# Kernel tuning notes

Hardware: AMD Instinct MI355X
Metric: run time of the kernel (lower is better)

## Reference

```python
import jax, jax.numpy as jnp
import numpy as np

N = 50000          # nodes
E = 800000         # edges (before self-loops)
IN_DIM = 128
HID = 64           # hidden_dim (per-head out channels)
HEADS = 2
NL = 3             # num_layers of GATConv
CH = HEADS * HID   # 128, per-layer node feature width
LSTM_H = (2 * CH) // 2  # 128, PyG JumpingKnowledge lstm hidden size (num_layers=2)
NEG_SLOPE = 0.2


def setup_inputs() -> dict:
    key = jax.random.key(0)
    ks = jax.random.split(key, 24)
    r = lambda i, shape, s=0.1: jax.random.normal(ks[i], shape, dtype=jnp.float32) * s
    return {
        "x": jax.random.normal(ks[0], (N, IN_DIM), dtype=jnp.float32),
        "edge_index": jax.random.randint(ks[1], (2, E), 0, N),
        "W1": r(2, (CH, IN_DIM)),
        "att1_src": r(3, (HEADS, HID)),
        "att1_dst": r(4, (HEADS, HID)),
        "b1": r(5, (CH,)),
        "Ws": r(6, (NL - 1, CH, CH)),
        "atts_src": r(7, (NL - 1, HEADS, HID)),
        "atts_dst": r(8, (NL - 1, HEADS, HID)),
        "bs": r(9, (NL - 1, CH)),
        "lstm_Wih": r(10, (2, 4 * LSTM_H, CH)),
        "lstm_Whh": r(11, (2, 4 * LSTM_H, LSTM_H)),
        "lstm_bih": r(12, (2, 4 * LSTM_H)),
        "lstm_bhh": r(13, (2, 4 * LSTM_H)),
        "jk_att_w": r(14, (1, 2 * LSTM_H)),
        "jk_att_b": r(15, (1,)),
        "lin1_w": r(16, (HID, CH)),
        "lin1_b": r(17, (HID,)),
        "lin2_w": r(18, (HID, HID + IN_DIM)),
        "lin2_b": r(19, (HID,)),
        "out_w": r(20, (6, HID)),
        "out_b": r(21, (6,)),
    }


def _gat(x, src, dst, W, a_src, a_dst, b):
    # PyG GATConv: linear -> per-head attention logits -> segment softmax over
    # incoming edges -> weighted scatter-add -> concat heads + bias.
    xp = (x @ W.T).reshape(N, HEADS, HID)          # [N,H,C]
    es = jnp.sum(xp * a_src, -1)                   # [N,H]
    ed = jnp.sum(xp * a_dst, -1)                   # [N,H]
    e = jax.nn.leaky_relu(es[src] + ed[dst], NEG_SLOPE)  # [E,H]
    m = jax.ops.segment_max(e, dst, num_segments=N)
    ex = jnp.exp(e - m[dst])
    s = jax.ops.segment_sum(ex, dst, num_segments=N)
    alpha = ex / s[dst]                            # [E,H]
    out = jax.ops.segment_sum(xp[src] * alpha[..., None], dst, num_segments=N)
    return out.reshape(N, CH) + b


def _lstm_dir(seq, Wih, Whh, bih, bhh, reverse):
    # seq: [L, N, CH]; torch gate order (i, f, g, o)
    def step(carry, xt):
        h, c = carry
        g = xt @ Wih.T + bih + h @ Whh.T + bhh
        i, f, gg, o = jnp.split(g, 4, axis=-1)
        c = jax.nn.sigmoid(f) * c + jax.nn.sigmoid(i) * jnp.tanh(gg)
        h = jax.nn.sigmoid(o) * jnp.tanh(c)
        return (h, c), h
    z = jnp.zeros((seq.shape[1], LSTM_H), seq.dtype)
    _, hs = jax.lax.scan(step, (z, z), seq, reverse=reverse)
    return hs  # [L, N, LSTM_H]


def reference(x, edge_index, W1, att1_src, att1_dst, b1, Ws, atts_src, atts_dst, bs,
              lstm_Wih, lstm_Whh, lstm_bih, lstm_bhh, jk_att_w, jk_att_b,
              lin1_w, lin1_b, lin2_w, lin2_b, out_w, out_b):
    loops = jnp.arange(N)
    src = jnp.concatenate([edge_index[0], loops])  # PyG adds self-loops
    dst = jnp.concatenate([edge_index[1], loops])

    h = _gat(x, src, dst, W1, att1_src, att1_dst, b1)  # conv1: no relu on xs[0]
    xs = [h]
    for l in range(NL - 1):
        h = jax.nn.relu(_gat(h, src, dst, Ws[l], atts_src[l], atts_dst[l], bs[l]))
        xs.append(h)

    # JumpingKnowledge 'lstm': biLSTM over layer axis, attention-weighted sum.
    X = jnp.stack(xs, axis=0)                       # [L, N, CH]
    hf = _lstm_dir(X, lstm_Wih[0], lstm_Whh[0], lstm_bih[0], lstm_bhh[0], False)
    hb = _lstm_dir(X, lstm_Wih[1], lstm_Whh[1], lstm_bih[1], lstm_bhh[1], True)
    hcat = jnp.concatenate([hf, hb], -1)            # [L, N, 2*LSTM_H]
    score = (hcat @ jk_att_w.T + jk_att_b)[..., 0]  # [L, N]
    alpha = jax.nn.softmax(score, axis=0)
    jk = jnp.sum(X * alpha[..., None], axis=0)      # [N, CH]

    h1 = jax.nn.relu(jk @ lin1_w.T + lin1_b)        # dropout is identity (eval)
    h2 = jax.nn.relu(jnp.concatenate([h1, x], axis=1) @ lin2_w.T + lin2_b)
    logits = h2 @ out_w.T + out_b
    return jax.nn.log_softmax(logits, axis=1)
```

## Files before the change

### kernel.cpp

```cpp
#include <hip/hip_runtime.h>
#include <math.h>

#define CDIV(a,b) (((a)+(b)-1)/(b))

typedef __attribute__((ext_vector_type(8))) short bfrag;
typedef __attribute__((ext_vector_type(4))) float ffrag;

__device__ inline unsigned short f2bf(float f) {
    unsigned int u = __float_as_uint(f);
    return (unsigned short)((u + 0x7fffu + ((u >> 16) & 1u)) >> 16);
}
__device__ inline float bf2f(unsigned short u) {
    return __uint_as_float(((unsigned int)u) << 16);
}
__device__ inline float sigf(float x) {
    return __builtin_amdgcn_rcpf(1.f + __expf(-x));
}
__device__ inline float tanhfast(float x) {
    float t = __expf(-2.f * fabsf(x));
    float r = (1.f - t) * __builtin_amdgcn_rcpf(1.f + t);
    return copysignf(r, x);
}
__device__ inline int hoff(int row, int k) {
    int sw = ((k >> 3) ^ row) & 15;
    return row * 128 + sw * 8 + (k & 7);
}

__global__ void zero_i32(int* __restrict__ p, int n) {
    int i = blockIdx.x * 256 + threadIdx.x;
    if (i < n) p[i] = 0;
}
__global__ void init_score_k(float* __restrict__ sc, const float* __restrict__ b, int n) {
    int i = blockIdx.x * 256 + threadIdx.x;
    if (i < n) sc[i] = b[0];
}
__global__ void convert_bf_k(const float* __restrict__ src, unsigned short* __restrict__ dst, int n) {
    int i = blockIdx.x * 256 + threadIdx.x;
    if (i < n) dst[i] = f2bf(src[i]);
}

__global__ void hist_k(const int* __restrict__ ei, int E, int ET, int* __restrict__ deg) {
    int e = blockIdx.x * 256 + threadIdx.x;
    if (e >= ET) return;
    int d = (e < E) ? ei[E + e] : e - E;
    atomicAdd(deg + d, 1);
}

__global__ __launch_bounds__(256)
void scan1_k(const int* __restrict__ deg, int* __restrict__ row_ptr,
             int* __restrict__ part, int Nn) {
    __shared__ int ls[256];
    int t = threadIdx.x;
    int base = blockIdx.x * 1024 + t * 4;
    int v[4];
    #pragma unroll
    for (int j = 0; j < 4; ++j) v[j] = (base + j < Nn) ? deg[base + j] : 0;
    int s = v[0] + v[1] + v[2] + v[3];
    ls[t] = s;
    __syncthreads();
    for (int off = 1; off < 256; off <<= 1) {
        int o = (t >= off) ? ls[t - off] : 0;
        __syncthreads();
        ls[t] += o;
        __syncthreads();
    }
    int run = ls[t] - s;
    if (t == 255) part[blockIdx.x] = ls[255];
    #pragma unroll
    for (int j = 0; j < 4; ++j) {
        if (base + j < Nn) row_ptr[base + j] = run;
        run += v[j];
    }
}
__global__ void scan2_k(int* __restrict__ part, int nb) {
    int lane = threadIdx.x;
    int v = (lane < nb) ? part[lane] : 0;
    int orig = v;
    for (int off = 1; off < 64; off <<= 1) {
        int o = __shfl_up(v, off);
        if (lane >= off) v += o;
    }
    if (lane < nb) part[lane] = v - orig;
}
__global__ void scan3_k(const int* __restrict__ part, int* __restrict__ row_ptr,
                        int* __restrict__ cursor, int Nn) {
    int i = blockIdx.x * 256 + threadIdx.x;
    if (i >= Nn) return;
    int v = row_ptr[i] + part[i >> 10];
    row_ptr[i] = v;
    cursor[i] = v;
}

__global__ void fill_k(const int* __restrict__ ei, int E, int ET,
                       int* __restrict__ cursor, int* __restrict__ csr_src) {
    int e = blockIdx.x * 256 + threadIdx.x;
    if (e >= ET) return;
    int s, d;
    if (e < E) { s = ei[e]; d = ei[E + e]; } else { s = e - E; d = s; }
    int pos = atomicAdd(cursor + d, 1);
    csr_src[pos] = s;
}

__global__ void pack_w_k(const float* __restrict__ Wih, const float* __restrict__ Whh,
                         const float* __restrict__ bih, const float* __restrict__ bhh,
                         unsigned short* __restrict__ Wp, float* __restrict__ bsum) {
    int i = blockIdx.x * 256 + threadIdx.x;
    if (i < 1024) bsum[i] = bih[i] + bhh[i];
    if (i >= 2 * 512 * 256) return;
    int k = i & 255, j = (i >> 8) & 511, d = i >> 17;
    float v = (k < 128) ? Wih[((size_t)d * 512 + j) * 128 + k]
                        : Whh[((size_t)d * 512 + j) * 128 + (k - 128)];
    Wp[i] = f2bf(v);
}

__global__ void pack_wb_k(const float* __restrict__ W1, const float* __restrict__ Ws,
                          const float* __restrict__ l1w, const float* __restrict__ l2w,
                          unsigned short* __restrict__ wb) {
    int i = blockIdx.x * 256 + threadIdx.x;
    if (i >= 69632) return;
    float v;
    if (i < 16384)      v = W1[i];
    else if (i < 49152) v = Ws[i - 16384];
    else if (i < 57344) v = l1w[i - 49152];
    else                v = l2w[i - 57344];
    wb[i] = f2bf(v);
}

template<int NT, int K, int K1, bool RELU, bool FUSE, bool BFOUT>
__global__ __launch_bounds__(256)
void gemm_mfma_k(const unsigned short* __restrict__ A1, const unsigned short* __restrict__ A2,
                 int ldA2, const unsigned short* __restrict__ Wb, const float* __restrict__ bias,
                 unsigned short* __restrict__ Cb, float* __restrict__ Cf,
                 const float* __restrict__ asl, const float* __restrict__ adl,
                 float* __restrict__ es, float* __restrict__ ed, int M)
{
    int tid = threadIdx.x;
    int wv = tid >> 6, lane = tid & 63;
    int col = lane & 15, kg = lane >> 4;
    int row0 = blockIdx.x * 64 + wv * 16;
    int mrow = row0 + col;
    bool mok = mrow < M;

    ffrag acc[NT];
    #pragma unroll
    for (int t = 0; t < NT; ++t) acc[t] = (ffrag){0.f, 0.f, 0.f, 0.f};

    #pragma unroll
    for (int ks = 0; ks < K / 32; ++ks) {
        int kk = ks * 32 + kg * 8;
        bfrag a = (bfrag){0,0,0,0,0,0,0,0};
        if (mok) {
            if (kk < K1) a = *(const bfrag*)(A1 + (size_t)mrow * K1 + kk);
            else         a = *(const bfrag*)(A2 + (size_t)mrow * ldA2 + (kk - K1));
        }
        #pragma unroll
        for (int t = 0; t < NT; ++t) {
            bfrag b = *(const bfrag*)(Wb + (size_t)(t * 16 + col) * K + kk);
            acc[t] = __builtin_amdgcn_mfma_f32_16x16x32_bf16(a, b, acc[t], 0, 0, 0);
        }
    }

    #pragma unroll
    for (int r = 0; r < 4; ++r) {
        int n = row0 + kg * 4 + r;
        bool ok = n < M;
        float e0 = 0.f, e1 = 0.f, d0 = 0.f, d1 = 0.f;
        #pragma unroll
        for (int t = 0; t < NT; ++t) {
            float v = acc[t][r];
            if (FUSE) {
                int ch = t * 16 + col;
                if (t < NT / 2) { e0 = fmaf(v, asl[ch], e0); d0 = fmaf(v, adl[ch], d0); }
                else            { e1 = fmaf(v, asl[ch], e1); d1 = fmaf(v, adl[ch], d1); }
            }
            if (bias) v += bias[t * 16 + col];
            if (RELU) v = fmaxf(v, 0.f);
            if (ok) {
                if (BFOUT) Cb[(size_t)n * (NT * 16) + t * 16 + col] = f2bf(v);
                else       Cf[(size_t)n * (NT * 16) + t * 16 + col] = v;
            }
        }
        if (FUSE) {
            #pragma unroll
            for (int mk = 1; mk < 16; mk <<= 1) {
                e0 += __shfl_xor(e0, mk); e1 += __shfl_xor(e1, mk);
                d0 += __shfl_xor(d0, mk); d1 += __shfl_xor(d1, mk);
            }
            if (col == 0 && ok) {
                es[n * 2] = e0; es[n * 2 + 1] = e1;
                ed[n * 2] = d0; ed[n * 2 + 1] = d1;
            }
        }
    }
}

__global__ __launch_bounds__(256)
void gat_agg_k(const int* __restrict__ csr_src, const int* __restrict__ row_ptr,
               const int* __restrict__ deg,
               const unsigned short* __restrict__ xpb, const float* __restrict__ es,
               const float* __restrict__ ed, const float* __restrict__ bias,
               unsigned short* __restrict__ out, int Nn, int relu)
{
    int wid = (blockIdx.x * 256 + threadIdx.x) >> 6;
    int lane = threadIdx.x & 63;
    if (wid >= Nn) return;
    int n = wid;
    int beg = row_ptr[n];
    int dn = deg[n];
    float2 edv = *(const float2*)(ed + n * 2);

    int   src_c = 0;
    float z0_c = 0.f, z1_c = 0.f;
    float m0 = -3e38f, m1 = -3e38f, s0 = 0.f, s1 = 0.f;
    for (int i = lane; i < dn; i += 64) {
        int s = csr_src[beg + i];
        float2 e2 = *(const float2*)(es + s * 2);
        float z0 = e2.x + edv.x; z0 = z0 > 0.f ? z0 : 0.2f * z0;
        float z1 = e2.y + edv.y; z1 = z1 > 0.f ? z1 : 0.2f * z1;
        if (i == lane) { src_c = s; z0_c = z0; z1_c = z1; }
        float nm0 = fmaxf(m0, z0);
        s0 = s0 * __expf(m0 - nm0) + __expf(z0 - nm0); m0 = nm0;
        float nm1 = fmaxf(m1, z1);
        s1 = s1 * __expf(m1 - nm1) + __expf(z1 - nm1); m1 = nm1;
    }
    #pragma unroll
    for (int off = 32; off; off >>= 1) {
        float om0 = __shfl_xor(m0, off), os0 = __shfl_xor(s0, off);
        float nm0 = fmaxf(m0, om0);
        s0 = s0 * __expf(m0 - nm0) + os0 * __expf(om0 - nm0); m0 = nm0;
        float om1 = __shfl_xor(m1, off), os1 = __shfl_xor(s1, off);
        float nm1 = fmaxf(m1, om1);
        s1 = s1 * __expf(m1 - nm1) + os1 * __expf(om1 - nm1); m1 = nm1;
    }
    float inv0 = 1.f / s0, inv1 = 1.f / s1;

    float acc0 = 0.f, acc1 = 0.f;
    if (dn <= 64) {
        #pragma unroll 8
        for (int i = 0; i < dn; ++i) {
            int s = __shfl(src_c, i);
            float a0 = __expf(__shfl(z0_c, i) - m0) * inv0;
            float a1 = __expf(__shfl(z1_c, i) - m1) * inv1;
            float aw = (lane < 32) ? a0 : a1;
            unsigned int u = *(const unsigned int*)(xpb + (size_t)s * 128 + 2 * lane);
            acc0 = fmaf(bf2f((unsigned short)(u & 0xffff)), aw, acc0);
            acc1 = fmaf(bf2f((unsigned short)(u >> 16)), aw, acc1);
        }
    } else {
        for (int i = 0; i < dn; ++i) {
            int s = csr_src[beg + i];
            float2 e2 = *(const float2*)(es + s * 2);
            float z0 = e2.x + edv.x; z0 = z0 > 0.f ? z0 : 0.2f * z0;
            float z1 = e2.y + edv.y; z1 = z1 > 0.f ? z1 : 0.2f * z1;
            float a0 = __expf(z0 - m0) * inv0;
            float a1 = __expf(z1 - m1) * inv1;
            float aw = (lane < 32) ? a0 : a1;
            unsigned int u = *(const unsigned int*)(xpb + (size_t)s * 128 + 2 * lane);
            acc0 = fmaf(bf2f((unsigned short)(u & 0xffff)), aw, acc0);
            acc1 = fmaf(bf2f((unsigned short)(u >> 16)), aw, acc1);
        }
    }
    float2 bb = *(const float2*)(bias + 2 * lane);
    float v0 = acc0 + bb.x;
    float v1 = acc1 + bb.y;
    if (relu) { v0 = fmaxf(v0, 0.f); v1 = fmaxf(v1, 0.f); }
    unsigned int o = (unsigned int)f2bf(v0) | ((unsigned int)f2bf(v1) << 16);
    *(unsigned int*)(out + (size_t)n * 128 + 2 * lane) = o;
}

__global__ __launch_bounds__(512)
void lstm_all_k(const unsigned short* __restrict__ X0, const unsigned short* __restrict__ X1,
                const unsigned short* __restrict__ X2,
                const unsigned short* __restrict__ WpB, const float* __restrict__ bsumB,
                const float* __restrict__ jkw, float* __restrict__ score, int Nn, int ntiles)
{
    __shared__ unsigned short h_lds[2][32 * 128];
    int dir = blockIdx.y;
    const unsigned short* Xs0 = dir ? X2 : X0;
    const unsigned short* Xs2 = dir ? X0 : X2;
    const unsigned short* Wp = WpB + (size_t)dir * 512 * 256;
    const float* bsum = bsumB + dir * 512;
    const float* wsc = jkw + dir * 128;

    int tid = threadIdx.x;
    int wv = tid >> 6, lane = tid & 63;
    int col = lane & 15, kg = lane >> 4;
    int t0 = dir ? 2 : 0;
    int kch = 16 * wv + col;
    float bi = bsum[kch], bf_ = bsum[128 + kch];
    float bg = bsum[256 + kch], bo = bsum[384 + kch];
    float wk = wsc[kch];

    bfrag wreg[4][8];
    #pragma unroll
    for (int g = 0; g < 4; ++g) {
        const unsigned short* wrow = Wp + (size_t)(16 * (8 * g + wv) + col) * 256;
        #pragma unroll
        for (int ks = 0; ks < 8; ++ks)
            wreg[g][ks] = *(const bfrag*)(wrow + ks * 32 + kg * 8);
    }

    for (int tile = blockIdx.x; tile < ntiles; tile += gridDim.x) {
        int node0 = tile * 32;
        float c[2][4] = {};

        #pragma unroll
        for (int i = 0; i < 3; ++i) {
            int t = (i == 0) ? t0 : ((i == 1) ? 1 : (2 - t0));
            const unsigned short* Xt = (i == 0) ? Xs0 : ((i == 1) ? X1 : Xs2);
            const unsigned short* h_rd = h_lds[(i + 1) & 1];
            unsigned short* h_wr = h_lds[i & 1];

            ffrag acc[2][4];
            #pragma unroll
            for (int nt = 0; nt < 2; ++nt)
                #pragma unroll
                for (int g = 0; g < 4; ++g) acc[nt][g] = (ffrag){0.f, 0.f, 0.f, 0.f};

            #pragma unroll
            for (int ks = 0; ks < 4; ++ks) {
                int kk = ks * 32 + kg * 8;
                bfrag a0 = *(const bfrag*)(Xt + (size_t)(node0 + col) * 128 + kk);
                bfrag a1 = *(const bfrag*)(Xt + (size_t)(node0 + 16 + col) * 128 + kk);
                #pragma unroll
                for (int g = 0; g < 4; ++g) {
                    acc[0][g] = __builtin_amdgcn_mfma_f32_16x16x32_bf16(a0, wreg[g][ks], acc[0][g], 0, 0, 0);
                    acc[1][g] = __builtin_amdgcn_mfma_f32_16x16x32_bf16(a1, wreg[g][ks], acc[1][g], 0, 0, 0);
                }
            }

            if (i > 0) {
                #pragma unroll
                for (int ks = 4; ks < 8; ++ks) {
                    int kh = (ks - 4) * 32 + kg * 8;
                    bfrag ah0 = *(const bfrag*)&h_rd[hoff(col, kh)];
                    bfrag ah1 = *(const bfrag*)&h_rd[hoff(16 + col, kh)];
                    #pragma unroll
                    for (int g = 0; g < 4; ++g) {
                        acc[0][g] = __builtin_amdgcn_mfma_f32_16x16x32_bf16(ah0, wreg[g][ks], acc[0][g], 0, 0, 0);
                        acc[1][g] = __builtin_amdgcn_mfma_f32_16x16x32_bf16(ah1, wreg[g][ks], acc[1][g], 0, 0, 0);
                    }
                }
            }

            #pragma unroll
            for (int nt = 0; nt < 2; ++nt) {
                #pragma unroll
                for (int r = 0; r < 4; ++r) {
                    float gi = acc[nt][0][r] + bi;
                    float gf = acc[nt][1][r] + bf_;
                    float gg = acc[nt][2][r] + bg;
                    float go = acc[nt][3][r] + bo;
                    float si = sigf(gi);
                    float sf = sigf(gf);
                    float so = sigf(go);
                    float tg = tanhfast(gg);
                    float cn = sf * c[nt][r] + si * tg;
                    float hn = so * tanhfast(cn);
                    c[nt][r] = cn;
                    int nl = nt * 16 + kg * 4 + r;
                    h_wr[hoff(nl, kch)] = f2bf(hn);
                    float v = hn * wk;
                    #pragma unroll
                    for (int mk = 1; mk < 16; mk <<= 1) v += __shfl_xor(v, mk);
                    if (col == 0) {
                        int n = node0 + nl;
                        if (n < Nn) atomicAdd(&score[(size_t)t * Nn + n], v);
                    }
                }
            }
            __syncthreads();
        }
    }
}

__global__ void jk_combine_k(const float* __restrict__ score, const unsigned short* __restrict__ x0,
                             const unsigned short* __restrict__ x1, const unsigned short* __restrict__ x2,
                             unsigned short* __restrict__ jkb, int N_) {
    int gid = blockIdx.x * 256 + threadIdx.x;
    int n = gid >> 5;
    if (n >= N_) return;
    int c = (gid & 31) * 4;
    float s0 = score[n], s1 = score[N_ + n], s2 = score[2*N_ + n];
    float mx = fmaxf(s0, fmaxf(s1, s2));
    float e0 = __expf(s0 - mx), e1 = __expf(s1 - mx), e2 = __expf(s2 - mx);
    float inv = 1.f / (e0 + e1 + e2);
    float a0 = e0 * inv, a1 = e1 * inv, a2 = e2 * inv;
    size_t off = (size_t)n * 128 + c;
    ushort4 u0 = *(const ushort4*)(x0 + off);
    ushort4 u1 = *(const ushort4*)(x1 + off);
    ushort4 u2 = *(const ushort4*)(x2 + off);
    ushort4 o;
    o.x = f2bf(a0*bf2f(u0.x) + a1*bf2f(u1.x) + a2*bf2f(u2.x));
    o.y = f2bf(a0*bf2f(u0.y) + a1*bf2f(u1.y) + a2*bf2f(u2.y));
    o.z = f2bf(a0*bf2f(u0.z) + a1*bf2f(u1.z) + a2*bf2f(u2.z));
    o.w = f2bf(a0*bf2f(u0.w) + a1*bf2f(u1.w) + a2*bf2f(u2.w));
    *(ushort4*)(jkb + off) = o;
}

__global__ void final_out_k(const float* __restrict__ h2, const float* __restrict__ ow,
                            const float* __restrict__ ob, float* __restrict__ out, int N_) {
    int n = blockIdx.x * 256 + threadIdx.x;
    if (n >= N_) return;
    float l[6];
    #pragma unroll
    for (int j = 0; j < 6; ++j) l[j] = ob[j];
    for (int c = 0; c < 64; c += 4) {
        float4 h4 = *(const float4*)(h2 + (size_t)n * 64 + c);
        #pragma unroll
        for (int j = 0; j < 6; ++j) {
            l[j] += h4.x * ow[j*64 + c + 0] + h4.y * ow[j*64 + c + 1]
                  + h4.z * ow[j*64 + c + 2] + h4.w * ow[j*64 + c + 3];
        }
    }
    float mx = l[0];
    #pragma unroll
    for (int j = 1; j < 6; ++j) mx = fmaxf(mx, l[j]);
    float se = 0.f;
    #pragma unroll
    for (int j = 0; j < 6; ++j) se += __expf(l[j] - mx);
    float ls = logf(se) + mx;
    #pragma unroll
    for (int j = 0; j < 6; ++j) out[(size_t)n * 6 + j] = l[j] - ls;
}

extern "C" void kernel_launch(void* const* d_in, const int* in_sizes, int n_in,
                              void* d_out, int out_size, void* d_ws, size_t ws_size,
                              hipStream_t stream) {
    const float* x   = (const float*)d_in[0];
    const int*   ei  = (const int*)d_in[1];
    const float* W1  = (const float*)d_in[2];
    const float* a1s = (const float*)d_in[3];
    const float* a1d = (const float*)d_in[4];
    const float* b1  = (const float*)d_in[5];
    const float* Ws  = (const float*)d_in[6];
    const float* ass = (const float*)d_in[7];
    const float* asd = (const float*)d_in[8];
    const float* bs  = (const float*)d_in[9];
    const float* Wih = (const float*)d_in[10];
    const float* Whh = (const float*)d_in[11];
    const float* bih = (const float*)d_in[12];
    const float* bhh = (const float*)d_in[13];
    const float* jkw = (const float*)d_in[14];
    const float* jkb_b = (const float*)d_in[15];
    const float* l1w = (const float*)d_in[16];
    const float* l1b = (const float*)d_in[17];
    const float* l2w = (const float*)d_in[18];
    const float* l2b = (const float*)d_in[19];
    const float* ow  = (const float*)d_in[20];
    const float* ob  = (const float*)d_in[21];
    float* out = (float*)d_out;

    int Nn = in_sizes[0] / 128;
    int E  = in_sizes[1] / 2;
    int ET = E + Nn;
    size_t Np = ((size_t)Nn + 63) & ~(size_t)63;
    size_t Fp = Np * 128;

    float* w = (float*)d_ws;
    float* es    = w;
    float* ed    = es + 2*Nn;
    float* score = ed + 2*Nn;
    float* bsum  = score + 3*Nn;
    float* h2    = bsum + 1024;
    unsigned short* xb   = (unsigned short*)(h2 + (size_t)Nn*64);
    unsigned short* xpb  = xb + Fp;
    unsigned short* xsb0 = xpb + Fp;
    unsigned short* xsb1 = xsb0 + Fp;
    unsigned short* xsb2 = xsb1 + Fp;
    unsigned short* h1b  = xsb2 + Fp;
    unsigned short* Wp   = h1b + Fp;
    unsigned short* wb   = Wp + 2*512*256;
    int* deg     = (int*)(wb + 69632);
    int* row_ptr = deg + Nn;
    int* cursor  = row_ptr + Nn;
    int* part    = cursor + Nn;
    int* csr_src = part + 64;
    unsigned short* jkb = xpb;

    int nb1 = CDIV(Nn, 1024);
    zero_i32<<<CDIV(Nn, 256), 256, 0, stream>>>(deg, Nn);
    hist_k<<<CDIV(ET, 256), 256, 0, stream>>>(ei, E, ET, deg);
    scan1_k<<<nb1, 256, 0, stream>>>(deg, row_ptr, part, Nn);
    scan2_k<<<1, 64, 0, stream>>>(part, nb1);
    scan3_k<<<CDIV(Nn, 256), 256, 0, stream>>>(part, row_ptr, cursor, Nn);
    fill_k<<<CDIV(ET, 256), 256, 0, stream>>>(ei, E, ET, cursor, csr_src);

    pack_w_k<<<CDIV(2*512*256, 256), 256, 0, stream>>>(Wih, Whh, bih, bhh, Wp, bsum);
    pack_wb_k<<<CDIV(69632, 256), 256, 0, stream>>>(W1, Ws, l1w, l2w, wb);
    convert_bf_k<<<CDIV(Nn*128, 256), 256, 0, stream>>>(x, xb, Nn*128);

    unsigned short* xsb_arr[3] = {xsb0, xsb1, xsb2};
    int gblk = CDIV(Nn, 64);

    for (int l = 0; l < 3; ++l) {
        const float* asl = (l == 0) ? a1s : ass + (size_t)(l-1) * 128;
        const float* adl = (l == 0) ? a1d : asd + (size_t)(l-1) * 128;
        const float* bl  = (l == 0) ? b1  : bs  + (size_t)(l-1) * 128;
        const unsigned short* Ain = (l == 0) ? xb : xsb_arr[l-1];
        const unsigned short* Wbl = wb + (size_t)l * 16384;
        gemm_mfma_k<8,128,128,false,true,true><<<gblk, 256, 0, stream>>>(
            Ain, Ain, 128, Wbl, nullptr, xpb, nullptr, asl, adl, es, ed, Nn);
        gat_agg_k<<<CDIV(Nn, 4), 256, 0, stream>>>(csr_src, row_ptr, deg, xpb, es, ed, bl,
                                                   xsb_arr[l], Nn, l > 0);
    }

    init_score_k<<<CDIV(3*Nn, 256), 256, 0, stream>>>(score, jkb_b, 3*Nn);
    int ntiles = CDIV(Nn, 32);
    int gx = ntiles < 128 ? ntiles : 128;
    lstm_all_k<<<dim3(gx, 2), 512, 0, stream>>>(xsb0, xsb1, xsb2, Wp, bsum, jkw, score, Nn, ntiles);

    jk_combine_k<<<CDIV(Nn*32, 256), 256, 0, stream>>>(score, xsb0, xsb1, xsb2, jkb, Nn);
    gemm_mfma_k<4,128,128,true,false,true><<<gblk, 256, 0, stream>>>(
        jkb, jkb, 128, wb + 49152, l1b, h1b, nullptr, nullptr, nullptr, nullptr, nullptr, Nn);
    gemm_mfma_k<4,192,64,true,false,false><<<gblk, 256, 0, stream>>>(
        h1b, xb, 128, wb + 57344, l2b, nullptr, h2, nullptr, nullptr, nullptr, nullptr, Nn);
    final_out_k<<<CDIV(Nn, 256), 256, 0, stream>>>(h2, ow, ob, out, Nn);
}
```

Measured before the change: 623.1 us.

## Fuse prep kernels, hoist attention exp out of aggregation loop, widen LSTM grid

Three unrelated changes. The weight packing and input bf16 conversion kernels are merged into one launch to cut launch overhead. In the low-degree GAT aggregation path, each lane computes its own attention weight once and the loop broadcasts it with shuffles, replacing a per-edge exp on every lane. The LSTM grid x-dimension cap rises from 128 to 256 blocks so more tiles run concurrently.

```diff
diff --git a/kernel.cpp b/kernel.cpp
--- a/kernel.cpp
+++ b/kernel.cpp
@@ -34,9 +34,35 @@
     int i = blockIdx.x * 256 + threadIdx.x;
     if (i < n) sc[i] = b[0];
 }
-__global__ void convert_bf_k(const float* __restrict__ src, unsigned short* __restrict__ dst, int n) {
+
+__global__ void prep_k(const float* __restrict__ Wih, const float* __restrict__ Whh,
+                       const float* __restrict__ bih, const float* __restrict__ bhh,
+                       unsigned short* __restrict__ Wp, float* __restrict__ bsum,
+                       const float* __restrict__ W1, const float* __restrict__ Ws,
+                       const float* __restrict__ l1w, const float* __restrict__ l2w,
+                       unsigned short* __restrict__ wb,
+                       const float* __restrict__ x, unsigned short* __restrict__ xb, int nx) {
     int i = blockIdx.x * 256 + threadIdx.x;
-    if (i < n) dst[i] = f2bf(src[i]);
+    if (i < 1024) bsum[i] = bih[i] + bhh[i];
+    if (i < 262144) {
+        int k = i & 255, j = (i >> 8) & 511, d = i >> 17;
+        float v = (k < 128) ? Wih[((size_t)d * 512 + j) * 128 + k]
+                            : Whh[((size_t)d * 512 + j) * 128 + (k - 128)];
+        Wp[i] = f2bf(v);
+        return;
+    }
+    int i2 = i - 262144;
+    if (i2 < 69632) {
+        float v;
+        if (i2 < 16384)      v = W1[i2];
+        else if (i2 < 49152) v = Ws[i2 - 16384];
+        else if (i2 < 57344) v = l1w[i2 - 49152];
+        else                 v = l2w[i2 - 57344];
+        wb[i2] = f2bf(v);
+        return;
+    }
+    int i3 = i2 - 69632;
+    if (i3 < nx) xb[i3] = f2bf(x[i3]);
 }
 
 __global__ void hist_k(const int* __restrict__ ei, int E, int ET, int* __restrict__ deg) {
@@ -99,31 +125,6 @@
     if (e < E) { s = ei[e]; d = ei[E + e]; } else { s = e - E; d = s; }
     int pos = atomicAdd(cursor + d, 1);
     csr_src[pos] = s;
-}
-
-__global__ void pack_w_k(const float* __restrict__ Wih, const float* __restrict__ Whh,
-                         const float* __restrict__ bih, const float* __restrict__ bhh,
-                         unsigned short* __restrict__ Wp, float* __restrict__ bsum) {
-    int i = blockIdx.x * 256 + threadIdx.x;
-    if (i < 1024) bsum[i] = bih[i] + bhh[i];
-    if (i >= 2 * 512 * 256) return;
-    int k = i & 255, j = (i >> 8) & 511, d = i >> 17;
-    float v = (k < 128) ? Wih[((size_t)d * 512 + j) * 128 + k]
-                        : Whh[((size_t)d * 512 + j) * 128 + (k - 128)];
-    Wp[i] = f2bf(v);
-}
-
-__global__ void pack_wb_k(const float* __restrict__ W1, const float* __restrict__ Ws,
-                          const float* __restrict__ l1w, const float* __restrict__ l2w,
-                          unsigned short* __restrict__ wb) {
-    int i = blockIdx.x * 256 + threadIdx.x;
-    if (i >= 69632) return;
-    float v;
-    if (i < 16384)      v = W1[i];
-    else if (i < 49152) v = Ws[i - 16384];
-    else if (i < 57344) v = l1w[i - 49152];
-    else                v = l2w[i - 57344];
-    wb[i] = f2bf(v);
 }
 
 template<int NT, int K, int K1, bool RELU, bool FUSE, bool BFOUT>
@@ -236,11 +237,13 @@
 
     float acc0 = 0.f, acc1 = 0.f;
     if (dn <= 64) {
+        float a0_c = __expf(z0_c - m0) * inv0;
+        float a1_c = __expf(z1_c - m1) * inv1;
         #pragma unroll 8
         for (int i = 0; i < dn; ++i) {
             int s = __shfl(src_c, i);
-            float a0 = __expf(__shfl(z0_c, i) - m0) * inv0;
-            float a1 = __expf(__shfl(z1_c, i) - m1) * inv1;
+            float a0 = __shfl(a0_c, i);
+            float a1 = __shfl(a1_c, i);
             float aw = (lane < 32) ? a0 : a1;
             unsigned int u = *(const unsigned int*)(xpb + (size_t)s * 128 + 2 * lane);
             acc0 = fmaf(bf2f((unsigned short)(u & 0xffff)), aw, acc0);
@@ -486,9 +489,9 @@
     scan3_k<<<CDIV(Nn, 256), 256, 0, stream>>>(part, row_ptr, cursor, Nn);
     fill_k<<<CDIV(ET, 256), 256, 0, stream>>>(ei, E, ET, cursor, csr_src);
 
-    pack_w_k<<<CDIV(2*512*256, 256), 256, 0, stream>>>(Wih, Whh, bih, bhh, Wp, bsum);
-    pack_wb_k<<<CDIV(69632, 256), 256, 0, stream>>>(W1, Ws, l1w, l2w, wb);
-    convert_bf_k<<<CDIV(Nn*128, 256), 256, 0, stream>>>(x, xb, Nn*128);
+    int nprep = 262144 + 69632 + Nn * 128;
+    prep_k<<<CDIV(nprep, 256), 256, 0, stream>>>(Wih, Whh, bih, bhh, Wp, bsum,
+                                                 W1, Ws, l1w, l2w, wb, x, xb, Nn * 128);
 
     unsigned short* xsb_arr[3] = {xsb0, xsb1, xsb2};
     int gblk = CDIV(Nn, 64);
@@ -507,7 +510,7 @@
 
     init_score_k<<<CDIV(3*Nn, 256), 256, 0, stream>>>(score, jkb_b, 3*Nn);
     int ntiles = CDIV(Nn, 32);
-    int gx = ntiles < 128 ? ntiles : 128;
+    int gx = ntiles < 256 ? ntiles : 256;
     lstm_all_k<<<dim3(gx, 2), 512, 0, stream>>>(xsb0, xsb1, xsb2, Wp, bsum, jkw, score, Nn, ntiles);
 
     jk_combine_k<<<CDIV(Nn*32, 256), 256, 0, stream>>>(score, xsb0, xsb1, xsb2, jkb, Nn);
```

Result: no change. 627.6 us (+0.7%).
